# Kernel tuning notes

Measured on AMD Instinct MI355X. Metric: run time of the kernel, lower is better.

Reference implementation:

```python
import jax, jax.numpy as jnp
import numpy as np

L, C, H, FF = 12, 768, 12, 3072
DH = C // H
VOCAB = 30522
B, P, T = 64, 196, 40
PATCH_FLAT = 768  # 16*16*3
MAXP, MAXW = P + 1, T + 2


def _ln(x, w, b, eps):
    m = jnp.mean(x, axis=-1, keepdims=True)
    v = jnp.mean(jnp.square(x - m), axis=-1, keepdims=True)
    return (x - m) * jax.lax.rsqrt(v + eps) * w + b


def setup_inputs() -> dict:
    key = jax.random.key(0)
    ks = iter(jax.random.split(key, 40))
    s = 0.02
    rn = lambda shape: jax.random.normal(next(ks), shape, jnp.float32) * s
    return {
        'vis_in': jax.random.normal(next(ks), (B, P, PATCH_FLAT), jnp.float32),
        'txt_in': jax.random.randint(next(ks), (B, T), 0, VOCAB),
        'vis_mask': jnp.ones((B, P), jnp.int32),
        'txt_mask': jnp.ones((B, T), jnp.int32),
        'patch_w': rn((C, PATCH_FLAT)), 'patch_b': jnp.zeros((C,), jnp.float32),
        'w_embed': rn((VOCAB, C)),
        't_pos': rn((MAXW, C)),
        'v_pos': rn((1, MAXP, C)),
        'v_cls': rn((1, 1, C)),
        'v_mod': rn((1, 1, C)), 't_mod': rn((1, 1, C)),
        'vn_w': jnp.ones((C,), jnp.float32), 'vn_b': jnp.zeros((C,), jnp.float32),
        'tn_w': jnp.ones((C,), jnp.float32), 'tn_b': jnp.zeros((C,), jnp.float32),
        'qkv_w': rn((L, 3 * C, C)), 'qkv_b': jnp.zeros((L, 3 * C), jnp.float32),
        'proj_w': rn((L, C, C)), 'proj_b': jnp.zeros((L, C), jnp.float32),
        'n1_w': jnp.ones((L, C), jnp.float32), 'n1_b': jnp.zeros((L, C), jnp.float32),
        'n2_w': jnp.ones((L, C), jnp.float32), 'n2_b': jnp.zeros((L, C), jnp.float32),
        'fc1_w': rn((L, FF, C)), 'fc1_b': jnp.zeros((L, FF), jnp.float32),
        'fc2_w': rn((L, C, FF)), 'fc2_b': jnp.zeros((L, C), jnp.float32),
    }


def reference(vis_in, txt_in, vis_mask, txt_mask, patch_w, patch_b, w_embed, t_pos,
              v_pos, v_cls, v_mod, t_mod, vn_w, vn_b, tn_w, tn_b, qkv_w, qkv_b,
              proj_w, proj_b, n1_w, n1_b, n2_w, n2_b, fc1_w, fc1_b, fc2_w, fc2_b):
    Bsz = vis_in.shape[0]
    # patch projection and word embedding
    v_emb = vis_in @ patch_w.T + patch_b                      # [B, P, C]
    t_emb = w_embed[txt_in]                                    # [B, T, C]
    v_emb = jnp.concatenate([jnp.broadcast_to(v_cls, (Bsz, 1, C)), v_emb], axis=1)
    VL = v_emb.shape[1]                                        # P + 1
    v_emb = _ln(v_emb + v_pos[:, :VL] + v_mod, vn_w, vn_b, 1e-5)
    t_emb = _ln(t_emb + t_pos[:T] + t_mod, tn_w, tn_b, 1e-5)
    x = jnp.concatenate([t_emb, v_emb], axis=1)                # [B, N, C], N = T+1+P
    m = jnp.concatenate([txt_mask, jnp.ones((Bsz, 1), txt_mask.dtype), vis_mask], axis=-1)
    # pairwise mask: attn_mask[b,i,j] == 0 -> masked (broadcast over heads)
    masked = (m[:, None, :, None] * m[:, None, None, :]) == 0  # [B,1,N,N]
    scale = DH ** -0.5
    for l in range(L):
        h = _ln(x, n1_w[l], n1_b[l], 1e-6)
        qkv = (h @ qkv_w[l].T + qkv_b[l]).reshape(Bsz, -1, 3, H, DH)
        q = jnp.transpose(qkv[:, :, 0], (0, 2, 1, 3))          # [B,H,N,DH]
        k = jnp.transpose(qkv[:, :, 1], (0, 2, 1, 3))
        v = jnp.transpose(qkv[:, :, 2], (0, 2, 1, 3))
        attn = jnp.einsum('bhqd,bhkd->bhqk', q, k) * scale
        attn = jnp.where(masked, jnp.asarray(-1e30, attn.dtype), attn)
        attn = jax.nn.softmax(attn, axis=-1)
        o = jnp.einsum('bhqk,bhkd->bhqd', attn, v)
        o = jnp.transpose(o, (0, 2, 1, 3)).reshape(Bsz, -1, C)
        x = x + (o @ proj_w[l].T + proj_b[l])
        h2 = _ln(x, n2_w[l], n2_b[l], 1e-6)
        h2 = jax.nn.gelu(h2 @ fc1_w[l].T + fc1_b[l], approximate=False)
        x = x + (h2 @ fc2_w[l].T + fc2_b[l])
    return x
```

## Files before the change

kernel.cpp:

```cpp
#include <hip/hip_runtime.h>
#include <hip/hip_bf16.h>

using bf16 = __hip_bfloat16;
typedef __bf16 bfv8 __attribute__((ext_vector_type(8)));
typedef float f32x4 __attribute__((ext_vector_type(4)));

#define DEVI __device__ __forceinline__

constexpr int L_ = 12, C_ = 768, H_ = 12, FF_ = 3072, DH_ = 64;
constexpr int B_ = 64, P_ = 196, T_ = 40;
constexpr int N_ = T_ + 1 + P_;
constexpr int M_ = B_ * N_;
constexpr int MPAD = 15232;
constexpr int NKV = 256;
constexpr int BP_ = B_ * P_;

constexpr size_t OFF_X   = 0;
constexpr size_t SZ_X    = (size_t)MPAD * C_ * 4;
constexpr size_t OFF_H   = OFF_X + SZ_X;
constexpr size_t SZ_H    = (size_t)MPAD * C_ * 2;
constexpr size_t OFF_Q   = OFF_H + SZ_H;
constexpr size_t SZ_QKV1 = (size_t)B_ * H_ * NKV * DH_ * 2;
constexpr size_t OFF_K   = OFF_Q + SZ_QKV1;
constexpr size_t OFF_V   = OFF_K + SZ_QKV1;
constexpr size_t OFF_P   = OFF_V + SZ_QKV1;
constexpr size_t SZ_P    = (size_t)B_ * H_ * NKV * NKV * 2;
constexpr size_t OFF_O   = OFF_P + SZ_P;
constexpr size_t SZ_O    = SZ_H;
constexpr size_t OFF_FFH = OFF_O + SZ_O;
constexpr size_t SZ_FFH  = (size_t)MPAD * FF_ * 2;
constexpr size_t OFF_WB  = OFF_FFH + SZ_FFH;
constexpr size_t SZ_WB   = (size_t)(2304 + 768 + 3072 + 3072) * 768 * 2;
constexpr size_t WS_NEED = OFF_WB + SZ_WB;
constexpr size_t OFF_PTMP = OFF_FFH;
constexpr size_t OFF_VISB = OFF_P;
constexpr size_t OFF_PWB  = OFF_WB;

DEVI bfv8 bfv8_zero() {
  union { int4 i; bfv8 v; } u; u.i = make_int4(0, 0, 0, 0); return u.v;
}

DEVI void gld_lds16(const bf16* g, bf16* l) {
  __builtin_amdgcn_global_load_lds((__attribute__((address_space(1))) void*)(g),
                                   (__attribute__((address_space(3))) void*)(l), 16, 0, 0);
}

DEVI void swz_tiles(int bid, int G, int NT, int& bm, int& bn) {
  const int qq = G >> 3, rr = G & 7;
  const int xcd = bid & 7, base = bid >> 3;
  const int lin = (xcd < rr ? xcd * (qq + 1) : rr * (qq + 1) + (xcd - rr) * qq) + base;
  bm = lin / NT;
  bn = lin - bm * NT;
}

__global__ __launch_bounds__(256) void conv_weights_k(
    const float* __restrict__ wq, const float* __restrict__ wp,
    const float* __restrict__ wf1, const float* __restrict__ wf2,
    bf16* __restrict__ dst) {
  const long n0 = 2304L * 768 / 4, n1 = 768L * 768 / 4;
  const long n2 = 3072L * 768 / 4, n3 = 3072L * 768 / 4;
  const long tot = n0 + n1 + n2 + n3;
  for (long i = (long)blockIdx.x * 256 + threadIdx.x; i < tot; i += (long)gridDim.x * 256) {
    const float* s; long off;
    if (i < n0) { s = wq; off = i; }
    else if (i < n0 + n1) { s = wp; off = i - n0; }
    else if (i < n0 + n1 + n2) { s = wf1; off = i - n0 - n1; }
    else { s = wf2; off = i - n0 - n1 - n2; }
    float4 v = ((const float4*)s)[off];
    union { short4 q; bf16 h[4]; } u;
    u.h[0] = __float2bfloat16(v.x); u.h[1] = __float2bfloat16(v.y);
    u.h[2] = __float2bfloat16(v.z); u.h[3] = __float2bfloat16(v.w);
    ((short4*)dst)[i] = u.q;
  }
}

__global__ __launch_bounds__(256) void f32_to_bf16_k(const float* __restrict__ s,
                                                     bf16* __restrict__ d, long n4) {
  long i = (long)blockIdx.x * 256 + threadIdx.x;
  long stride = (long)gridDim.x * 256;
  for (; i < n4; i += stride) {
    float4 v = ((const float4*)s)[i];
    union { short4 q; bf16 h[4]; } u;
    u.h[0] = __float2bfloat16(v.x); u.h[1] = __float2bfloat16(v.y);
    u.h[2] = __float2bfloat16(v.z); u.h[3] = __float2bfloat16(v.w);
    ((short4*)d)[i] = u.q;
  }
}

template <int EPI>
__global__ __launch_bounds__(256) void gemm_bt(
    const bf16* __restrict__ A, const bf16* __restrict__ W,
    const float* __restrict__ bias, float* __restrict__ outf,
    float* __restrict__ outf2, bf16* __restrict__ outb, bf16* __restrict__ qb,
    bf16* __restrict__ kb, bf16* __restrict__ vb, int Nout, int K, int Mvalid,
    int NT) {
  __shared__ alignas(16) bf16 As[128 * 32];
  __shared__ alignas(16) bf16 Bs[128 * 32];
  const int tid = threadIdx.x;
  const int wid = tid >> 6, lane = tid & 63;
  const int wm = wid >> 1, wn = wid & 1;
  int bm, bn;
  swz_tiles(blockIdx.x, gridDim.x, NT, bm, bn);
  const size_t arow0 = (size_t)bm * 128;
  const size_t brow0 = (size_t)bn * 128;

  f32x4 acc[4][4];
#pragma unroll
  for (int m = 0; m < 4; m++)
#pragma unroll
    for (int n = 0; n < 4; n++) acc[m][n] = (f32x4){0.f, 0.f, 0.f, 0.f};

  const int c0 = tid,        r0 = c0 >> 2, cb0 = (c0 & 3) * 8;
  const int c1 = tid + 256,  r1 = c1 >> 2, cb1 = (c1 & 3) * 8;
  bf16* asb0 = As + (size_t)(wid * 64) * 8;
  bf16* asb1 = As + (size_t)(wid * 64 + 256) * 8;
  bf16* bsb0 = Bs + (size_t)(wid * 64) * 8;
  bf16* bsb1 = Bs + (size_t)(wid * 64 + 256) * 8;

  for (int k0 = 0; k0 < K; k0 += 32) {
    gld_lds16(A + (arow0 + r0) * K + k0 + cb0, asb0);
    gld_lds16(A + (arow0 + r1) * K + k0 + cb1, asb1);
    gld_lds16(W + (brow0 + r0) * K + k0 + cb0, bsb0);
    gld_lds16(W + (brow0 + r1) * K + k0 + cb1, bsb1);
    asm volatile("s_waitcnt vmcnt(0)" ::: "memory");
    __syncthreads();
    bfv8 af[4], bfr[4];
#pragma unroll
    for (int m = 0; m < 4; m++)
      af[m] = *(const bfv8*)&As[(wm * 64 + m * 16 + (lane & 15)) * 32 + (lane >> 4) * 8];
#pragma unroll
    for (int n = 0; n < 4; n++)
      bfr[n] = *(const bfv8*)&Bs[(wn * 64 + n * 16 + (lane & 15)) * 32 + (lane >> 4) * 8];
#pragma unroll
    for (int m = 0; m < 4; m++)
#pragma unroll
      for (int n = 0; n < 4; n++)
        acc[m][n] = __builtin_amdgcn_mfma_f32_16x16x32_bf16(af[m], bfr[n], acc[m][n], 0, 0, 0);
    __syncthreads();
  }

  const int row0 = (int)arow0 + wm * 64;
  const int col0 = (int)brow0 + wn * 64;
#pragma unroll
  for (int n = 0; n < 4; n++) {
    const int colb = col0 + n * 16 + (lane & 15);
    const float bv = bias[colb];
#pragma unroll
    for (int m = 0; m < 4; m++) {
#pragma unroll
      for (int j = 0; j < 4; j++) {
        const int row = row0 + m * 16 + (lane >> 4) * 4 + j;
        const float v = acc[m][n][j] + bv;
        if constexpr (EPI == 0) {
          outf[(size_t)row * Nout + colb] = v;
        } else if constexpr (EPI == 1) {
          if (row < Mvalid) {
            const int bI = row / N_;
            const int nI = row - bI * N_;
            const int s = colb / C_;
            const int rem = colb - s * C_;
            const int hh = rem >> 6, dd = rem & 63;
            bf16* dst = (s == 0) ? qb : (s == 1) ? kb : vb;
            dst[(((size_t)bI * H_ + hh) * NKV + nI) * DH_ + dd] = __float2bfloat16(v);
          }
        } else if constexpr (EPI == 2) {
          outf[(size_t)row * Nout + colb] += v;
        } else if constexpr (EPI == 3) {
          const float g = 0.5f * v * (1.f + erff(v * 0.70710678118f));
          outb[(size_t)row * Nout + colb] = __float2bfloat16(g);
        } else {
          if (row < Mvalid)
            outf2[(size_t)row * Nout + colb] = outf[(size_t)row * Nout + colb] + v;
        }
      }
    }
  }
}

__global__ __launch_bounds__(256) void embed_kernel(
    const float* __restrict__ ptmp, const int* __restrict__ txt_in,
    const float* __restrict__ wemb, const float* __restrict__ tpos,
    const float* __restrict__ vpos, const float* __restrict__ vcls,
    const float* __restrict__ vmod, const float* __restrict__ tmod,
    const float* __restrict__ vnw, const float* __restrict__ vnb,
    const float* __restrict__ tnw, const float* __restrict__ tnb,
    float* __restrict__ x) {
  const int row = blockIdx.x;
  const int tid = threadIdx.x;
  if (row >= M_) {
    for (int i = tid; i < C_; i += 256) x[(size_t)row * C_ + i] = 0.f;
    return;
  }
  const int b = row / N_, n = row - (row / N_) * N_;
  const bool istxt = n < T_;
  float e[3];
#pragma unroll
  for (int i = 0; i < 3; i++) {
    const int c = tid + i * 256;
    float v;
    if (istxt) {
      v = wemb[(size_t)txt_in[b * T_ + n] * C_ + c] + tpos[n * C_ + c] + tmod[c];
    } else {
      const int vi = n - T_;
      const float base = (vi == 0) ? vcls[c] : ptmp[((size_t)b * P_ + (vi - 1)) * C_ + c];
      v = base + vpos[vi * C_ + c] + vmod[c];
    }
    e[i] = v;
  }
  float s = e[0] + e[1] + e[2];
  float s2 = e[0] * e[0] + e[1] * e[1] + e[2] * e[2];
#pragma unroll
  for (int d = 1; d < 64; d <<= 1) { s += __shfl_xor(s, d); s2 += __shfl_xor(s2, d); }
  __shared__ float rs[4], rs2[4];
  const int wid = tid >> 6, lane = tid & 63;
  if (lane == 0) { rs[wid] = s; rs2[wid] = s2; }
  __syncthreads();
  s = rs[0] + rs[1] + rs[2] + rs[3];
  s2 = rs2[0] + rs2[1] + rs2[2] + rs2[3];
  const float mean = s * (1.f / C_);
  const float var = s2 * (1.f / C_) - mean * mean;
  const float rr = rsqrtf(var + 1e-5f);
  const float* w = istxt ? tnw : vnw;
  const float* bb = istxt ? tnb : vnb;
#pragma unroll
  for (int i = 0; i < 3; i++) {
    const int c = tid + i * 256;
    x[(size_t)row * C_ + c] = (e[i] - mean) * rr * w[c] + bb[c];
  }
}

__global__ __launch_bounds__(256) void ln_rows(const float* __restrict__ x,
                                               const float* __restrict__ w,
                                               const float* __restrict__ b,
                                               bf16* __restrict__ out, float eps) {
  const int row = blockIdx.x * 4 + (threadIdx.x >> 6);
  const int lane = threadIdx.x & 63;
  if (row >= MPAD) return;
  bf16* op = out + (size_t)row * C_;
  if (row >= M_) {
#pragma unroll
    for (int i = 0; i < 3; i++)
      *(short4*)(op + (lane + 64 * i) * 4) = make_short4(0, 0, 0, 0);
    return;
  }
  const float4* xp = (const float4*)(x + (size_t)row * C_);
  float4 v[3];
  float s = 0.f, s2 = 0.f;
#pragma unroll
  for (int i = 0; i < 3; i++) {
    v[i] = xp[lane + 64 * i];
    s += v[i].x + v[i].y + v[i].z + v[i].w;
    s2 += v[i].x * v[i].x + v[i].y * v[i].y + v[i].z * v[i].z + v[i].w * v[i].w;
  }
#pragma unroll
  for (int d = 1; d < 64; d <<= 1) { s += __shfl_xor(s, d); s2 += __shfl_xor(s2, d); }
  const float mean = s * (1.f / C_);
  const float rr = rsqrtf(s2 * (1.f / C_) - mean * mean + eps);
#pragma unroll
  for (int i = 0; i < 3; i++) {
    const int c0 = (lane + 64 * i) * 4;
    const float4 w4 = *(const float4*)(w + c0);
    const float4 b4 = *(const float4*)(b + c0);
    union { short4 s4; bf16 h[4]; } u;
    u.h[0] = __float2bfloat16((v[i].x - mean) * rr * w4.x + b4.x);
    u.h[1] = __float2bfloat16((v[i].y - mean) * rr * w4.y + b4.y);
    u.h[2] = __float2bfloat16((v[i].z - mean) * rr * w4.z + b4.z);
    u.h[3] = __float2bfloat16((v[i].w - mean) * rr * w4.w + b4.w);
    *(short4*)(op + c0) = u.s4;
  }
}

DEVI float maskval(const int* __restrict__ tm, const int* __restrict__ vm, int b, int j) {
  if (j < T_) return tm[b * T_ + j] ? 1.f : 0.f;
  if (j == T_) return 1.f;
  if (j < N_) return vm[b * P_ + (j - T_ - 1)] ? 1.f : 0.f;
  return 0.f;
}

__global__ __launch_bounds__(256) void attn_fused(
    const bf16* __restrict__ qb, const bf16* __restrict__ kb,
    const bf16* __restrict__ vb, const int* __restrict__ txt_mask,
    const int* __restrict__ vis_mask, bf16* __restrict__ ob) {
  __shared__ alignas(16) __bf16 Vt[64 * 264];
  __shared__ alignas(16) __bf16 Ps[64 * 264];
  const int qblk = blockIdx.x;
  const int bh = blockIdx.y;
  const int b = bh / H_, hh = bh - b * H_;
  const int tid = threadIdx.x, wid = tid >> 6, lane = tid & 63;

  const __bf16* Vg = (const __bf16*)(vb + (size_t)bh * NKV * DH_);
#pragma unroll
  for (int it = 0; it < 8; it++) {
    const int r = lane + 64 * (it & 3);
    const int c8 = (wid + 4 * (it >> 2)) * 8;
    bfv8 v;
    if (r < N_) v = *(const bfv8*)(Vg + (size_t)r * DH_ + c8);
    else { union { int4 i; bfv8 x; } z; z.i = make_int4(0,0,0,0); v = z.x; }
#pragma unroll
    for (int d = 0; d < 8; d++) Vt[(c8 + d) * 264 + r] = v[d];
  }

  const int qbase = qblk * 64 + wid * 16;
  const __bf16* Qg = (const __bf16*)(qb + (size_t)bh * NKV * DH_);
  const __bf16* Kg = (const __bf16*)(kb + (size_t)bh * NKV * DH_);
  bfv8 aq[2];
#pragma unroll
  for (int kk = 0; kk < 2; kk++)
    aq[kk] = *(const bfv8*)(Qg + (size_t)(qbase + (lane & 15)) * DH_ + kk * 32 + (lane >> 4) * 8);

  f32x4 acc[16];
#pragma unroll
  for (int f = 0; f < 16; f++) acc[f] = (f32x4){0.f, 0.f, 0.f, 0.f};
#pragma unroll
  for (int f = 0; f < 16; f++) {
#pragma unroll
    for (int kk = 0; kk < 2; kk++) {
      bfv8 bk = *(const bfv8*)(Kg + (size_t)(f * 16 + (lane & 15)) * DH_ + kk * 32 + (lane >> 4) * 8);
      acc[f] = __builtin_amdgcn_mfma_f32_16x16x32_bf16(aq[kk], bk, acc[f], 0, 0, 0);
    }
  }

  float cm[16];
#pragma unroll
  for (int f = 0; f < 16; f++)
    cm[f] = maskval(txt_mask, vis_mask, b, f * 16 + (lane & 15));

  const float scale = 0.125f;
#pragma unroll
  for (int j = 0; j < 4; j++) {
    const int qr = qbase + (lane >> 4) * 4 + j;
    const float qm = (qr < N_) ? maskval(txt_mask, vis_mask, b, qr) : 1.f;
    float sv[16];
    float mx = -3.0e38f;
#pragma unroll
    for (int f = 0; f < 16; f++) {
      const int col = f * 16 + (lane & 15);
      float sc;
      if (col >= N_) sc = -INFINITY;
      else if (qm * cm[f] == 0.f) sc = -1e30f;
      else sc = acc[f][j] * scale;
      sv[f] = sc;
      mx = fmaxf(mx, sc);
    }
#pragma unroll
    for (int d = 1; d < 16; d <<= 1) mx = fmaxf(mx, __shfl_xor(mx, d));
    float sum = 0.f;
#pragma unroll
    for (int f = 0; f < 16; f++) { const float p = expf(sv[f] - mx); sv[f] = p; sum += p; }
#pragma unroll
    for (int d = 1; d < 16; d <<= 1) sum += __shfl_xor(sum, d);
    const float inv = 1.f / sum;
    const int ql = wid * 16 + (lane >> 4) * 4 + j;
#pragma unroll
    for (int f = 0; f < 16; f++)
      Ps[ql * 264 + f * 16 + (lane & 15)] = (__bf16)(sv[f] * inv);
  }

  __syncthreads();

  f32x4 oacc[4];
#pragma unroll
  for (int n = 0; n < 4; n++) oacc[n] = (f32x4){0.f, 0.f, 0.f, 0.f};
#pragma unroll
  for (int kk = 0; kk < 8; kk++) {
    bfv8 ap = *(const bfv8*)&Ps[(wid * 16 + (lane & 15)) * 264 + kk * 32 + (lane >> 4) * 8];
#pragma unroll
    for (int n = 0; n < 4; n++) {
      bfv8 bv = *(const bfv8*)&Vt[(n * 16 + (lane & 15)) * 264 + kk * 32 + (lane >> 4) * 8];
      oacc[n] = __builtin_amdgcn_mfma_f32_16x16x32_bf16(ap, bv, oacc[n], 0, 0, 0);
    }
  }
#pragma unroll
  for (int n = 0; n < 4; n++)
#pragma unroll
    for (int j = 0; j < 4; j++) {
      const int q = qbase + (lane >> 4) * 4 + j;
      if (q < N_)
        ob[((size_t)b * N_ + q) * C_ + hh * 64 + n * 16 + (lane & 15)] =
            __float2bfloat16(oacc[n][j]);
    }
}

extern "C" void kernel_launch(void* const* d_in, const int* in_sizes, int n_in,
                              void* d_out, int out_size, void* d_ws, size_t ws_size,
                              hipStream_t stream) {
  const float* vis_in  = (const float*)d_in[0];
  const int*   txt_in  = (const int*)d_in[1];
  const int*   vis_mask = (const int*)d_in[2];
  const int*   txt_mask = (const int*)d_in[3];
  const float* patch_w = (const float*)d_in[4];
  const float* patch_b = (const float*)d_in[5];
  const float* w_embed = (const float*)d_in[6];
  const float* t_pos   = (const float*)d_in[7];
  const float* v_pos   = (const float*)d_in[8];
  const float* v_cls   = (const float*)d_in[9];
  const float* v_mod   = (const float*)d_in[10];
  const float* t_mod   = (const float*)d_in[11];
  const float* vn_w = (const float*)d_in[12];
  const float* vn_b = (const float*)d_in[13];
  const float* tn_w = (const float*)d_in[14];
  const float* tn_b = (const float*)d_in[15];
  const float* qkv_w = (const float*)d_in[16];
  const float* qkv_b = (const float*)d_in[17];
  const float* proj_w = (const float*)d_in[18];
  const float* proj_b = (const float*)d_in[19];
  const float* n1_w = (const float*)d_in[20];
  const float* n1_b = (const float*)d_in[21];
  const float* n2_w = (const float*)d_in[22];
  const float* n2_b = (const float*)d_in[23];
  const float* fc1_w = (const float*)d_in[24];
  const float* fc1_b = (const float*)d_in[25];
  const float* fc2_w = (const float*)d_in[26];
  const float* fc2_b = (const float*)d_in[27];

  char* ws = (char*)d_ws;
  if (ws_size < WS_NEED) {
    hipMemsetAsync(d_out, 0, (size_t)out_size * 4, stream);
    return;
  }
  float* x    = (float*)(ws + OFF_X);
  bf16* h     = (bf16*)(ws + OFF_H);
  bf16* qbuf  = (bf16*)(ws + OFF_Q);
  bf16* kbuf  = (bf16*)(ws + OFF_K);
  bf16* vbuf  = (bf16*)(ws + OFF_V);
  bf16* obuf  = (bf16*)(ws + OFF_O);
  bf16* ffh   = (bf16*)(ws + OFF_FFH);
  bf16* wq    = (bf16*)(ws + OFF_WB);
  bf16* wp    = wq + (size_t)2304 * 768;
  bf16* wf1   = wp + (size_t)768 * 768;
  bf16* wf2   = wf1 + (size_t)3072 * 768;
  float* ptmp = (float*)(ws + OFF_PTMP);
  bf16* visb  = (bf16*)(ws + OFF_VISB);
  bf16* pwb   = (bf16*)(ws + OFF_PWB);

  f32_to_bf16_k<<<1024, 256, 0, stream>>>(vis_in, visb, (long)BP_ * C_ / 4);
  f32_to_bf16_k<<<256, 256, 0, stream>>>(patch_w, pwb, (long)C_ * C_ / 4);
  gemm_bt<0><<<(BP_ / 128) * (C_ / 128), 256, 0, stream>>>(
      visb, pwb, patch_b, ptmp, nullptr, nullptr, nullptr, nullptr, nullptr,
      C_, C_, BP_, C_ / 128);
  embed_kernel<<<MPAD, 256, 0, stream>>>(ptmp, txt_in, w_embed, t_pos, v_pos, v_cls,
                                         v_mod, t_mod, vn_w, vn_b, tn_w, tn_b, x);

  for (int l = 0; l < L_; l++) {
    conv_weights_k<<<2048, 256, 0, stream>>>(
        qkv_w + (size_t)l * 2304 * 768, proj_w + (size_t)l * 768 * 768,
        fc1_w + (size_t)l * 3072 * 768, fc2_w + (size_t)l * 768 * 3072, wq);

    ln_rows<<<MPAD / 4, 256, 0, stream>>>(x, n1_w + l * C_, n1_b + l * C_, h, 1e-6f);
    gemm_bt<1><<<(MPAD / 128) * (2304 / 128), 256, 0, stream>>>(
        h, wq, qkv_b + (size_t)l * 2304, nullptr, nullptr, nullptr, qbuf, kbuf, vbuf,
        2304, C_, M_, 2304 / 128);
    attn_fused<<<dim3(4, B_ * H_), 256, 0, stream>>>(qbuf, kbuf, vbuf, txt_mask,
                                                     vis_mask, obuf);
    gemm_bt<2><<<(MPAD / 128) * (C_ / 128), 256, 0, stream>>>(
        obuf, wp, proj_b + (size_t)l * C_, x, nullptr, nullptr, nullptr, nullptr,
        nullptr, C_, C_, M_, C_ / 128);
    ln_rows<<<MPAD / 4, 256, 0, stream>>>(x, n2_w + l * C_, n2_b + l * C_, h, 1e-6f);
    gemm_bt<3><<<(MPAD / 128) * (FF_ / 128), 256, 0, stream>>>(
        h, wf1, fc1_b + (size_t)l * FF_, nullptr, nullptr, ffh, nullptr, nullptr,
        nullptr, FF_, C_, M_, FF_ / 128);
    if (l < L_ - 1) {
      gemm_bt<2><<<(MPAD / 128) * (C_ / 128), 256, 0, stream>>>(
          ffh, wf2, fc2_b + (size_t)l * C_, x, nullptr, nullptr, nullptr, nullptr,
          nullptr, C_, FF_, M_, C_ / 128);
    } else {
      gemm_bt<4><<<(MPAD / 128) * (C_ / 128), 256, 0, stream>>>(
          ffh, wf2, fc2_b + (size_t)l * C_, x, (float*)d_out, nullptr, nullptr,
          nullptr, nullptr, C_, FF_, M_, C_ / 128);
    }
  }
}
```

Measured before the change: 6.464 ms.

## Replace GEMM with double-buffered swizzled-LDS kernel, larger tiles, packed epilogues

Replaces the single-buffered 128x128, K=32 GEMM with a templated kernel. It double-buffers 64-wide K tiles through LDS using async global-to-LDS loads and partial vmcnt waits, and XOR-swizzles LDS columns to avoid bank conflicts. The QKV and FC1 GEMMs move to 256x256 tiles with 512 threads. Epilogues pack bf16 pairs via lane shuffles, and exact erf GELU is replaced by a tanh-style exp2 approximation. M padding grows to a multiple of 256 and the unused P buffer is dropped, at the cost of more LDS per block and small GELU numeric differences.

```diff
diff --git a/kernel.cpp b/kernel.cpp
--- a/kernel.cpp
+++ b/kernel.cpp
@@ -11,7 +11,7 @@
 constexpr int B_ = 64, P_ = 196, T_ = 40;
 constexpr int N_ = T_ + 1 + P_;
 constexpr int M_ = B_ * N_;
-constexpr int MPAD = 15232;
+constexpr int MPAD = 15360;
 constexpr int NKV = 256;
 constexpr int BP_ = B_ * P_;
 
@@ -23,9 +23,7 @@
 constexpr size_t SZ_QKV1 = (size_t)B_ * H_ * NKV * DH_ * 2;
 constexpr size_t OFF_K   = OFF_Q + SZ_QKV1;
 constexpr size_t OFF_V   = OFF_K + SZ_QKV1;
-constexpr size_t OFF_P   = OFF_V + SZ_QKV1;
-constexpr size_t SZ_P    = (size_t)B_ * H_ * NKV * NKV * 2;
-constexpr size_t OFF_O   = OFF_P + SZ_P;
+constexpr size_t OFF_O   = OFF_V + SZ_QKV1;
 constexpr size_t SZ_O    = SZ_H;
 constexpr size_t OFF_FFH = OFF_O + SZ_O;
 constexpr size_t SZ_FFH  = (size_t)MPAD * FF_ * 2;
@@ -33,24 +31,179 @@
 constexpr size_t SZ_WB   = (size_t)(2304 + 768 + 3072 + 3072) * 768 * 2;
 constexpr size_t WS_NEED = OFF_WB + SZ_WB;
 constexpr size_t OFF_PTMP = OFF_FFH;
-constexpr size_t OFF_VISB = OFF_P;
+constexpr size_t OFF_VISB = OFF_FFH + (size_t)40 * 1024 * 1024;
 constexpr size_t OFF_PWB  = OFF_WB;
-
-DEVI bfv8 bfv8_zero() {
-  union { int4 i; bfv8 v; } u; u.i = make_int4(0, 0, 0, 0); return u.v;
-}
 
 DEVI void gld_lds16(const bf16* g, bf16* l) {
   __builtin_amdgcn_global_load_lds((__attribute__((address_space(1))) void*)(g),
                                    (__attribute__((address_space(3))) void*)(l), 16, 0, 0);
 }
 
-DEVI void swz_tiles(int bid, int G, int NT, int& bm, int& bn) {
+DEVI void swz_tiles(int bid, int G, int NTC, int& bm, int& bn) {
   const int qq = G >> 3, rr = G & 7;
   const int xcd = bid & 7, base = bid >> 3;
   const int lin = (xcd < rr ? xcd * (qq + 1) : rr * (qq + 1) + (xcd - rr) * qq) + base;
-  bm = lin / NT;
-  bn = lin - bm * NT;
+  bm = lin / NTC;
+  bn = lin - bm * NTC;
+}
+
+DEVI uint packbf(float lo, float hi) {
+  union { struct { bf16 x, y; } h; uint u; } r;
+  r.h.x = __float2bfloat16(lo); r.h.y = __float2bfloat16(hi);
+  return r.u;
+}
+
+DEVI float gelu_f(float v) {
+  const float p = v * (1.5957691f + 0.07135481f * v * v) * 1.442695041f;
+  const float d = exp2f(-p);
+  return v / (1.f + d);
+}
+
+template <int BM, int BN, int TPB, int WM, int WN, int EPI>
+__global__ __launch_bounds__(TPB, 2) void gemm2ph(
+    const bf16* __restrict__ A, const bf16* __restrict__ W,
+    const float* __restrict__ bias, float* __restrict__ outf,
+    float* __restrict__ outf2, bf16* __restrict__ outb,
+    bf16* __restrict__ qb, bf16* __restrict__ kb, bf16* __restrict__ vb,
+    int Nout, int K, int Mvalid, int NTC) {
+  extern __shared__ __align__(16) char lds[];
+  constexpr int NWAVE = TPB / 64;
+  constexpr int MR = BM / (WM * 16);
+  constexpr int NR = BN / (WN * 16);
+  constexpr int LA = (BM / 8) / NWAVE;
+  constexpr int LB = (BN / 8) / NWAVE;
+  constexpr int TOTL = LA + LB;
+  constexpr int ASZ = BM * 128;
+  constexpr int BUF = ASZ + BN * 128;
+
+  const int tid = threadIdx.x, wid = tid >> 6, lane = tid & 63;
+  const int wm = wid / WN, wn = wid % WN;
+  int bm, bn;
+  swz_tiles(blockIdx.x, gridDim.x, NTC, bm, bn);
+  const size_t arow0 = (size_t)bm * BM;
+  const size_t brow0 = (size_t)bn * BN;
+
+  const int cswz = (((lane & 7) ^ ((lane >> 3) & 7)) * 8);
+  const size_t aoff0 = (arow0 + (size_t)wid * (LA * 8) + (lane >> 3)) * K + cswz;
+  const size_t boff0 = (brow0 + (size_t)wid * (LB * 8) + (lane >> 3)) * K + cswz;
+
+  f32x4 acc[MR][NR];
+#pragma unroll
+  for (int m = 0; m < MR; m++)
+#pragma unroll
+    for (int n = 0; n < NR; n++) acc[m][n] = (f32x4){0.f, 0.f, 0.f, 0.f};
+
+  auto STAGE = [&](int t, int bufoff) {
+    const size_t ka = aoff0 + (size_t)t * 64;
+#pragma unroll
+    for (int i = 0; i < LA; i++)
+      gld_lds16(A + ka + (size_t)i * 8 * K,
+                (bf16*)(lds + bufoff + (wid * LA + i) * 1024));
+    const size_t kw = boff0 + (size_t)t * 64;
+#pragma unroll
+    for (int i = 0; i < LB; i++)
+      gld_lds16(W + kw + (size_t)i * 8 * K,
+                (bf16*)(lds + bufoff + ASZ + (wid * LB + i) * 1024));
+  };
+
+  const int la = lane & 15, g = lane >> 4, s7 = lane & 7;
+  auto COMPUTE = [&](int bufoff) {
+    const char* Ab = lds + bufoff;
+    const char* Bb = lds + bufoff + ASZ;
+#pragma unroll
+    for (int ks = 0; ks < 2; ks++) {
+      const int slot = ((ks * 4 + g) ^ s7) * 16;
+      bfv8 bfr[NR];
+#pragma unroll
+      for (int n = 0; n < NR; n++)
+        bfr[n] = *(const bfv8*)(Bb + (wn * (NR * 16) + n * 16 + la) * 128 + slot);
+#pragma unroll
+      for (int m = 0; m < MR; m++) {
+        bfv8 af = *(const bfv8*)(Ab + (wm * (MR * 16) + m * 16 + la) * 128 + slot);
+#pragma unroll
+        for (int n = 0; n < NR; n++)
+          acc[m][n] = __builtin_amdgcn_mfma_f32_16x16x32_bf16(af, bfr[n], acc[m][n], 0, 0, 0);
+      }
+    }
+  };
+
+  const int NT = K >> 6;
+  STAGE(0, 0);
+  int cur = 0;
+  for (int t = 0; t < NT; ++t) {
+    if (t + 1 < NT) {
+      STAGE(t + 1, (cur ^ 1) * BUF);
+      if constexpr (TOTL == 8) asm volatile("s_waitcnt vmcnt(8)" ::: "memory");
+      else if constexpr (TOTL == 6) asm volatile("s_waitcnt vmcnt(6)" ::: "memory");
+      else asm volatile("s_waitcnt vmcnt(4)" ::: "memory");
+    } else {
+      asm volatile("s_waitcnt vmcnt(0)" ::: "memory");
+    }
+    asm volatile("s_barrier" ::: "memory");
+    COMPUTE(cur * BUF);
+    asm volatile("s_barrier" ::: "memory");
+    cur ^= 1;
+  }
+
+  const int row0 = (int)arow0 + wm * (MR * 16);
+  const int col0 = (int)brow0 + wn * (NR * 16);
+  float bv[NR];
+#pragma unroll
+  for (int n = 0; n < NR; n++) bv[n] = bias[col0 + n * 16 + la];
+
+  if constexpr (EPI == 0 || EPI == 2 || EPI == 4) {
+#pragma unroll
+    for (int n = 0; n < NR; n++) {
+      const int colb = col0 + n * 16 + la;
+#pragma unroll
+      for (int m = 0; m < MR; m++)
+#pragma unroll
+        for (int j = 0; j < 4; j++) {
+          const int row = row0 + m * 16 + (lane >> 4) * 4 + j;
+          const float v = acc[m][n][j] + bv[n];
+          if constexpr (EPI == 0) outf[(size_t)row * Nout + colb] = v;
+          else if constexpr (EPI == 2) outf[(size_t)row * Nout + colb] += v;
+          else { if (row < Mvalid) outf2[(size_t)row * Nout + colb] = outf[(size_t)row * Nout + colb] + v; }
+        }
+    }
+  } else if constexpr (EPI == 3) {
+#pragma unroll
+    for (int m = 0; m < MR; m++)
+#pragma unroll
+      for (int j = 0; j < 4; j++) {
+        const int row = row0 + m * 16 + (lane >> 4) * 4 + j;
+#pragma unroll
+        for (int n = 0; n < NR; n++) {
+          const float v = gelu_f(acc[m][n][j] + bv[n]);
+          const float p = __shfl_xor(v, 1);
+          if (!(lane & 1))
+            *(uint*)(outb + (size_t)row * Nout + col0 + n * 16 + la) = packbf(v, p);
+        }
+      }
+  } else {
+#pragma unroll
+    for (int m = 0; m < MR; m++)
+#pragma unroll
+      for (int j = 0; j < 4; j++) {
+        const int row = row0 + m * 16 + (lane >> 4) * 4 + j;
+        const bool ok = row < Mvalid;
+        const int bI = row / N_;
+        const int nI = row - bI * N_;
+#pragma unroll
+        for (int n = 0; n < NR; n++) {
+          const int colb = col0 + n * 16 + la;
+          const float v = acc[m][n][j] + bv[n];
+          const float p = __shfl_xor(v, 1);
+          if (ok && !(lane & 1)) {
+            const int s = colb / C_;
+            const int rem = colb - s * C_;
+            const int hh = rem >> 6, dd = rem & 63;
+            bf16* dst = (s == 0) ? qb : (s == 1) ? kb : vb;
+            *(uint*)(dst + (((size_t)bI * H_ + hh) * NKV + nI) * DH_ + dd) = packbf(v, p);
+          }
+        }
+      }
+  }
 }
 
 __global__ __launch_bounds__(256) void conv_weights_k(
@@ -58,8 +211,8 @@
     const float* __restrict__ wf1, const float* __restrict__ wf2,
     bf16* __restrict__ dst) {
   const long n0 = 2304L * 768 / 4, n1 = 768L * 768 / 4;
-  const long n2 = 3072L * 768 / 4, n3 = 3072L * 768 / 4;
-  const long tot = n0 + n1 + n2 + n3;
+  const long n2 = 3072L * 768 / 4;
+  const long tot = n0 + n1 + 2 * n2;
   for (long i = (long)blockIdx.x * 256 + threadIdx.x; i < tot; i += (long)gridDim.x * 256) {
     const float* s; long off;
     if (i < n0) { s = wq; off = i; }
@@ -84,96 +237,6 @@
     u.h[0] = __float2bfloat16(v.x); u.h[1] = __float2bfloat16(v.y);
     u.h[2] = __float2bfloat16(v.z); u.h[3] = __float2bfloat16(v.w);
     ((short4*)d)[i] = u.q;
-  }
-}
-
-template <int EPI>
-__global__ __launch_bounds__(256) void gemm_bt(
-    const bf16* __restrict__ A, const bf16* __restrict__ W,
-    const float* __restrict__ bias, float* __restrict__ outf,
-    float* __restrict__ outf2, bf16* __restrict__ outb, bf16* __restrict__ qb,
-    bf16* __restrict__ kb, bf16* __restrict__ vb, int Nout, int K, int Mvalid,
-    int NT) {
-  __shared__ alignas(16) bf16 As[128 * 32];
-  __shared__ alignas(16) bf16 Bs[128 * 32];
-  const int tid = threadIdx.x;
-  const int wid = tid >> 6, lane = tid & 63;
-  const int wm = wid >> 1, wn = wid & 1;
-  int bm, bn;
-  swz_tiles(blockIdx.x, gridDim.x, NT, bm, bn);
-  const size_t arow0 = (size_t)bm * 128;
-  const size_t brow0 = (size_t)bn * 128;
-
-  f32x4 acc[4][4];
-#pragma unroll
-  for (int m = 0; m < 4; m++)
-#pragma unroll
-    for (int n = 0; n < 4; n++) acc[m][n] = (f32x4){0.f, 0.f, 0.f, 0.f};
-
-  const int c0 = tid,        r0 = c0 >> 2, cb0 = (c0 & 3) * 8;
-  const int c1 = tid + 256,  r1 = c1 >> 2, cb1 = (c1 & 3) * 8;
-  bf16* asb0 = As + (size_t)(wid * 64) * 8;
-  bf16* asb1 = As + (size_t)(wid * 64 + 256) * 8;
-  bf16* bsb0 = Bs + (size_t)(wid * 64) * 8;
-  bf16* bsb1 = Bs + (size_t)(wid * 64 + 256) * 8;
-
-  for (int k0 = 0; k0 < K; k0 += 32) {
-    gld_lds16(A + (arow0 + r0) * K + k0 + cb0, asb0);
-    gld_lds16(A + (arow0 + r1) * K + k0 + cb1, asb1);
-    gld_lds16(W + (brow0 + r0) * K + k0 + cb0, bsb0);
-    gld_lds16(W + (brow0 + r1) * K + k0 + cb1, bsb1);
-    asm volatile("s_waitcnt vmcnt(0)" ::: "memory");
-    __syncthreads();
-    bfv8 af[4], bfr[4];
-#pragma unroll
-    for (int m = 0; m < 4; m++)
-      af[m] = *(const bfv8*)&As[(wm * 64 + m * 16 + (lane & 15)) * 32 + (lane >> 4) * 8];
-#pragma unroll
-    for (int n = 0; n < 4; n++)
-      bfr[n] = *(const bfv8*)&Bs[(wn * 64 + n * 16 + (lane & 15)) * 32 + (lane >> 4) * 8];
-#pragma unroll
-    for (int m = 0; m < 4; m++)
-#pragma unroll
-      for (int n = 0; n < 4; n++)
-        acc[m][n] = __builtin_amdgcn_mfma_f32_16x16x32_bf16(af[m], bfr[n], acc[m][n], 0, 0, 0);
-    __syncthreads();
-  }
-
-  const int row0 = (int)arow0 + wm * 64;
-  const int col0 = (int)brow0 + wn * 64;
-#pragma unroll
-  for (int n = 0; n < 4; n++) {
-    const int colb = col0 + n * 16 + (lane & 15);
-    const float bv = bias[colb];
-#pragma unroll
-    for (int m = 0; m < 4; m++) {
-#pragma unroll
-      for (int j = 0; j < 4; j++) {
-        const int row = row0 + m * 16 + (lane >> 4) * 4 + j;
-        const float v = acc[m][n][j] + bv;
-        if constexpr (EPI == 0) {
-          outf[(size_t)row * Nout + colb] = v;
-        } else if constexpr (EPI == 1) {
-          if (row < Mvalid) {
-            const int bI = row / N_;
-            const int nI = row - bI * N_;
-            const int s = colb / C_;
-            const int rem = colb - s * C_;
-            const int hh = rem >> 6, dd = rem & 63;
-            bf16* dst = (s == 0) ? qb : (s == 1) ? kb : vb;
-            dst[(((size_t)bI * H_ + hh) * NKV + nI) * DH_ + dd] = __float2bfloat16(v);
-          }
-        } else if constexpr (EPI == 2) {
-          outf[(size_t)row * Nout + colb] += v;
-        } else if constexpr (EPI == 3) {
-          const float g = 0.5f * v * (1.f + erff(v * 0.70710678118f));
-          outb[(size_t)row * Nout + colb] = __float2bfloat16(g);
-        } else {
-          if (row < Mvalid)
-            outf2[(size_t)row * Nout + colb] = outf[(size_t)row * Nout + colb] + v;
-        }
-      }
-    }
   }
 }
 
@@ -433,9 +496,23 @@
   bf16* visb  = (bf16*)(ws + OFF_VISB);
   bf16* pwb   = (bf16*)(ws + OFF_PWB);
 
+  constexpr int LDS_A = 2 * (256 + 256) * 128;
+  constexpr int LDS_B = 2 * (256 + 128) * 128;
+  constexpr int LDS_C = 2 * (128 + 128) * 128;
+  (void)hipFuncSetAttribute((const void*)gemm2ph<256, 256, 512, 2, 4, 1>,
+                            hipFuncAttributeMaxDynamicSharedMemorySize, LDS_A);
+  (void)hipFuncSetAttribute((const void*)gemm2ph<256, 256, 512, 2, 4, 3>,
+                            hipFuncAttributeMaxDynamicSharedMemorySize, LDS_A);
+  (void)hipFuncSetAttribute((const void*)gemm2ph<256, 128, 512, 2, 4, 0>,
+                            hipFuncAttributeMaxDynamicSharedMemorySize, LDS_B);
+  (void)hipFuncSetAttribute((const void*)gemm2ph<128, 128, 256, 2, 2, 2>,
+                            hipFuncAttributeMaxDynamicSharedMemorySize, LDS_C);
+  (void)hipFuncSetAttribute((const void*)gemm2ph<128, 128, 256, 2, 2, 4>,
+                            hipFuncAttributeMaxDynamicSharedMemorySize, LDS_C);
+
   f32_to_bf16_k<<<1024, 256, 0, stream>>>(vis_in, visb, (long)BP_ * C_ / 4);
   f32_to_bf16_k<<<256, 256, 0, stream>>>(patch_w, pwb, (long)C_ * C_ / 4);
-  gemm_bt<0><<<(BP_ / 128) * (C_ / 128), 256, 0, stream>>>(
+  gemm2ph<256, 128, 512, 2, 4, 0><<<(BP_ / 256) * (C_ / 128), 512, LDS_B, stream>>>(
       visb, pwb, patch_b, ptmp, nullptr, nullptr, nullptr, nullptr, nullptr,
       C_, C_, BP_, C_ / 128);
   embed_kernel<<<MPAD, 256, 0, stream>>>(ptmp, txt_in, w_embed, t_pos, v_pos, v_cls,
@@ -447,24 +524,24 @@
         fc1_w + (size_t)l * 3072 * 768, fc2_w + (size_t)l * 768 * 3072, wq);
 
     ln_rows<<<MPAD / 4, 256, 0, stream>>>(x, n1_w + l * C_, n1_b + l * C_, h, 1e-6f);
-    gemm_bt<1><<<(MPAD / 128) * (2304 / 128), 256, 0, stream>>>(
+    gemm2ph<256, 256, 512, 2, 4, 1><<<(MPAD / 256) * (2304 / 256), 512, LDS_A, stream>>>(
         h, wq, qkv_b + (size_t)l * 2304, nullptr, nullptr, nullptr, qbuf, kbuf, vbuf,
-        2304, C_, M_, 2304 / 128);
+        2304, C_, M_, 2304 / 256);
     attn_fused<<<dim3(4, B_ * H_), 256, 0, stream>>>(qbuf, kbuf, vbuf, txt_mask,
                                                      vis_mask, obuf);
-    gemm_bt<2><<<(MPAD / 128) * (C_ / 128), 256, 0, stream>>>(
+    gemm2ph<128, 128, 256, 2, 2, 2><<<(MPAD / 128) * (C_ / 128), 256, LDS_C, stream>>>(
         obuf, wp, proj_b + (size_t)l * C_, x, nullptr, nullptr, nullptr, nullptr,
         nullptr, C_, C_, M_, C_ / 128);
     ln_rows<<<MPAD / 4, 256, 0, stream>>>(x, n2_w + l * C_, n2_b + l * C_, h, 1e-6f);
-    gemm_bt<3><<<(MPAD / 128) * (FF_ / 128), 256, 0, stream>>>(
+    gemm2ph<256, 256, 512, 2, 4, 3><<<(MPAD / 256) * (FF_ / 256), 512, LDS_A, stream>>>(
         h, wf1, fc1_b + (size_t)l * FF_, nullptr, nullptr, ffh, nullptr, nullptr,
-        nullptr, FF_, C_, M_, FF_ / 128);
+        nullptr, FF_, C_, M_, FF_ / 256);
     if (l < L_ - 1) {
-      gemm_bt<2><<<(MPAD / 128) * (C_ / 128), 256, 0, stream>>>(
+      gemm2ph<128, 128, 256, 2, 2, 2><<<(MPAD / 128) * (C_ / 128), 256, LDS_C, stream>>>(
           ffh, wf2, fc2_b + (size_t)l * C_, x, nullptr, nullptr, nullptr, nullptr,
           nullptr, C_, FF_, M_, C_ / 128);
     } else {
-      gemm_bt<4><<<(MPAD / 128) * (C_ / 128), 256, 0, stream>>>(
+      gemm2ph<128, 128, 256, 2, 2, 4><<<(MPAD / 128) * (C_ / 128), 256, LDS_C, stream>>>(
           ffh, wf2, fc2_b + (size_t)l * C_, x, (float*)d_out, nullptr, nullptr,
           nullptr, nullptr, C_, FF_, M_, C_ / 128);
     }
```

New measurement: 6.410 ms. Within noise of the previous version (-0.8%).
